# Optimization experiments

Measured on AMD Instinct MI355X. Metric: run time of the kernel, lower is better.

The kernel has to match this reference:

```python
import jax, jax.numpy as jnp
import numpy as np

NUM_EMBEDDINGS = 8192
EMBEDDING_DIM = 512
COMMITMENT_COST = 0.25
N_INPUTS = 32768


def setup_inputs() -> dict:
    key = jax.random.key(0)
    k1, k2 = jax.random.split(key)
    inputs = jax.random.normal(k1, (N_INPUTS, EMBEDDING_DIM), dtype=jnp.float32)
    weight = jax.random.normal(k2, (NUM_EMBEDDINGS, EMBEDDING_DIM), dtype=jnp.float32)
    return {"inputs": inputs, "weight": weight}


def reference(inputs, weight):
    # distances[n, k] = ||x_n||^2 + ||w_k||^2 - 2 x_n . w_k   -> [N, K]
    distances = (
        jnp.sum(inputs ** 2, axis=1, keepdims=True)
        + jnp.sum(weight ** 2, axis=1)
        - 2.0 * (inputs @ weight.T)
    )
    probs = jax.nn.softmax(-distances, axis=-1)            # [N, K]
    idx = jnp.argmin(distances, axis=1)                    # [N]
    quantized = weight[idx]                                # gather == one-hot @ weight

    e_latent_loss = jnp.mean((jax.lax.stop_gradient(quantized) - inputs) ** 2)
    q_latent_loss = jnp.mean((quantized - jax.lax.stop_gradient(inputs)) ** 2)
    loss = q_latent_loss + COMMITMENT_COST * e_latent_loss

    # straight-through estimator
    quantized_st = inputs + jax.lax.stop_gradient(quantized - inputs)

    # avg over one-hot encodings == normalized code histogram
    counts = jnp.bincount(idx, length=NUM_EMBEDDINGS).astype(inputs.dtype)
    avg_probs = counts / inputs.shape[0]
    perplexity = jnp.exp(-jnp.sum(avg_probs * jnp.log(avg_probs + 1e-10)))

    return (quantized_st, probs, loss, perplexity)
```

## Files before the change

### kernel.cpp

```cpp
#include <hip/hip_runtime.h>
#include <hip/hip_fp16.h>
#include <math.h>

#define N_ROWS 32768
#define K_CODES 8192
#define DIM 512

#define OUT_Q 0
#define OUT_P ((size_t)N_ROWS * DIM)
#define OUT_LOSS (OUT_P + (size_t)N_ROWS * K_CODES)
#define OUT_PERP (OUT_LOSS + 1)

#define WS_WSQ 0
#define WS_CNT (K_CODES)
#define WS_ERR (2 * K_CODES)
#define WS_F16 (2 * K_CODES + N_ROWS)

#define XH_OFF ((size_t)0)
#define XL_OFF ((size_t)N_ROWS * DIM)
#define WH_OFF ((size_t)2 * N_ROWS * DIM)
#define WL_OFF ((size_t)2 * N_ROWS * DIM + (size_t)K_CODES * DIM)
#define F16_COUNT ((size_t)2 * (N_ROWS + K_CODES) * DIM)
#define WS_NEEDED ((size_t)WS_F16 * 4 + F16_COUNT * 2)

typedef _Float16 f16x8 __attribute__((ext_vector_type(8)));
typedef float f32x4 __attribute__((ext_vector_type(4)));

__device__ inline void load_lds16(const void* g, void* l) {
    __builtin_amdgcn_global_load_lds((const __attribute__((address_space(1))) void*)g,
                                     (__attribute__((address_space(3))) void*)l,
                                     16, 0, 0);
}

__device__ inline unsigned int fkey(float f) {
    unsigned int b = __float_as_uint(f);
    return b ^ ((unsigned int)((int)b >> 31) | 0x80000000u);
}
__device__ inline float fkey_inv(unsigned int k) {
    unsigned int b = (k & 0x80000000u) ? (k ^ 0x80000000u) : ~k;
    return __uint_as_float(b);
}

__global__ void wsq_kernel(const float* __restrict__ W, float* __restrict__ ws) {
    int row = blockIdx.x;
    int lane = threadIdx.x;
    const float* src = W + (size_t)row * DIM;
    float4 v0 = *(const float4*)(src + lane * 8);
    float4 v1 = *(const float4*)(src + lane * 8 + 4);
    float s = v0.x * v0.x + v0.y * v0.y + v0.z * v0.z + v0.w * v0.w
            + v1.x * v1.x + v1.y * v1.y + v1.z * v1.z + v1.w * v1.w;
#pragma unroll
    for (int off = 32; off > 0; off >>= 1) s += __shfl_down(s, off, 64);
    if (lane == 0) ws[WS_WSQ + row] = s;
}

__global__ void __launch_bounds__(256) convert_split_kernel(
    const float* __restrict__ X, const float* __restrict__ W,
    _Float16* __restrict__ f16base) {
    const size_t NX8 = (size_t)N_ROWS * DIM / 8;
    size_t t = (size_t)blockIdx.x * 256 + threadIdx.x;
    const float* src;
    _Float16 *hd, *ld;
    if (t < NX8) {
        src = X + t * 8;
        hd = f16base + XH_OFF + t * 8;
        ld = f16base + XL_OFF + t * 8;
    } else {
        size_t u = t - NX8;
        src = W + u * 8;
        hd = f16base + WH_OFF + u * 8;
        ld = f16base + WL_OFF + u * 8;
    }
    float4 v0 = *(const float4*)src;
    float4 v1 = *(const float4*)(src + 4);
    float v[8] = {v0.x, v0.y, v0.z, v0.w, v1.x, v1.y, v1.z, v1.w};
    f16x8 h, l;
#pragma unroll
    for (int i = 0; i < 8; ++i) {
        _Float16 hv = (_Float16)v[i];
        h[i] = hv;
        l[i] = (_Float16)(v[i] - (float)hv);
    }
    *(f16x8*)hd = h;
    *(f16x8*)ld = l;
}

__global__ void __launch_bounds__(256) gemm_dist_mfma_kernel(
    const _Float16* __restrict__ f16base, const float* __restrict__ ws,
    float* __restrict__ out) {
    __shared__ _Float16 lds[4][128][32];

    const int tid = threadIdx.x;
    const int w = tid >> 6;
    const int lane = tid & 63;
    const int bn = blockIdx.x * 128;
    const int bm = blockIdx.y * 128;
    const int wr = w >> 1;
    const int wc = w & 1;

    const _Float16* src_base;
    int tile_row_base;
    if (w == 0)      { src_base = f16base + XH_OFF; tile_row_base = bm; }
    else if (w == 1) { src_base = f16base + XL_OFF; tile_row_base = bm; }
    else if (w == 2) { src_base = f16base + WH_OFF; tile_row_base = bn; }
    else             { src_base = f16base + WL_OFF; tile_row_base = bn; }

    const int lrow = lane >> 2;
    const int p = lane & 3;

    f32x4 acc[4][4];
#pragma unroll
    for (int i = 0; i < 4; ++i)
#pragma unroll
        for (int j = 0; j < 4; ++j) acc[i][j] = (f32x4){0.f, 0.f, 0.f, 0.f};

    const int q = lane >> 4;
    const int fm = lane & 15;

    for (int k0 = 0; k0 < DIM; k0 += 32) {
        __syncthreads();
#pragma unroll
        for (int e = 0; e < 8; ++e) {
            int m = e * 16 + lrow;
            int c = p ^ ((m >> 1) & 3);
            const _Float16* gp =
                src_base + (size_t)(tile_row_base + m) * DIM + k0 + c * 8;
            load_lds16(gp, &lds[w][e * 16][0]);
        }
        __syncthreads();

        f16x8 ah[4], al[4], bh[4], bl[4];
#pragma unroll
        for (int i = 0; i < 4; ++i) {
            int am = wr * 64 + i * 16 + fm;
            int sa = (am >> 1) & 3;
            ah[i] = *(const f16x8*)&lds[0][am][(q ^ sa) * 8];
            al[i] = *(const f16x8*)&lds[1][am][(q ^ sa) * 8];
            int bb = wc * 64 + i * 16 + fm;
            int sb = (bb >> 1) & 3;
            bh[i] = *(const f16x8*)&lds[2][bb][(q ^ sb) * 8];
            bl[i] = *(const f16x8*)&lds[3][bb][(q ^ sb) * 8];
        }
#pragma unroll
        for (int i = 0; i < 4; ++i)
#pragma unroll
            for (int j = 0; j < 4; ++j) {
                acc[i][j] = __builtin_amdgcn_mfma_f32_16x16x32_f16(
                    ah[i], bh[j], acc[i][j], 0, 0, 0);
                acc[i][j] = __builtin_amdgcn_mfma_f32_16x16x32_f16(
                    ah[i], bl[j], acc[i][j], 0, 0, 0);
                acc[i][j] = __builtin_amdgcn_mfma_f32_16x16x32_f16(
                    al[i], bh[j], acc[i][j], 0, 0, 0);
            }
    }

    const float* wsq = ws + WS_WSQ;
    float* Dout = out + OUT_P;
    const int q4 = (lane >> 4) * 4;
#pragma unroll
    for (int i = 0; i < 4; ++i) {
#pragma unroll
        for (int j = 0; j < 4; ++j) {
            int n = bn + wc * 64 + j * 16 + fm;
            float wn = wsq[n];
#pragma unroll
            for (int r = 0; r < 4; ++r) {
                int m = bm + wr * 64 + i * 16 + q4 + r;
                Dout[(size_t)m * K_CODES + n] = wn - 2.f * acc[i][j][r];
            }
        }
    }
}

#define BM 128
#define BN 128
#define BK 16

__global__ void __launch_bounds__(256) gemm_dist_fp32_kernel(
    const float* __restrict__ X, const float* __restrict__ W,
    const float* __restrict__ ws, float* __restrict__ out) {
    __shared__ float As[BK][BM];
    __shared__ float Bs[BK][BN];

    const int bn = blockIdx.x * BN;
    const int bm = blockIdx.y * BM;
    const int tid = threadIdx.x;
    const int tx = tid & 15;
    const int ty = tid >> 4;
    const int lr = tid >> 1;
    const int lc = (tid & 1) * 8;

    float acc[8][8];
#pragma unroll
    for (int i = 0; i < 8; ++i)
#pragma unroll
        for (int j = 0; j < 8; ++j) acc[i][j] = 0.f;

    const float* aptr = X + (size_t)(bm + lr) * DIM + lc;
    const float* bptr = W + (size_t)(bn + lr) * DIM + lc;

    for (int k0 = 0; k0 < DIM; k0 += BK) {
        float4 a0 = *(const float4*)(aptr + k0);
        float4 a1 = *(const float4*)(aptr + k0 + 4);
        float4 b0 = *(const float4*)(bptr + k0);
        float4 b1 = *(const float4*)(bptr + k0 + 4);
        __syncthreads();
        As[lc + 0][lr] = a0.x; As[lc + 1][lr] = a0.y;
        As[lc + 2][lr] = a0.z; As[lc + 3][lr] = a0.w;
        As[lc + 4][lr] = a1.x; As[lc + 5][lr] = a1.y;
        As[lc + 6][lr] = a1.z; As[lc + 7][lr] = a1.w;
        Bs[lc + 0][lr] = b0.x; Bs[lc + 1][lr] = b0.y;
        Bs[lc + 2][lr] = b0.z; Bs[lc + 3][lr] = b0.w;
        Bs[lc + 4][lr] = b1.x; Bs[lc + 5][lr] = b1.y;
        Bs[lc + 6][lr] = b1.z; Bs[lc + 7][lr] = b1.w;
        __syncthreads();
#pragma unroll
        for (int kk = 0; kk < BK; ++kk) {
            float a[8], b[8];
            *(float4*)&a[0] = *(const float4*)&As[kk][ty * 8];
            *(float4*)&a[4] = *(const float4*)&As[kk][ty * 8 + 4];
            *(float4*)&b[0] = *(const float4*)&Bs[kk][tx * 8];
            *(float4*)&b[4] = *(const float4*)&Bs[kk][tx * 8 + 4];
#pragma unroll
            for (int i = 0; i < 8; ++i)
#pragma unroll
                for (int j = 0; j < 8; ++j)
                    acc[i][j] = fmaf(a[i], b[j], acc[i][j]);
        }
    }

    const float* wsq = ws + WS_WSQ;
    const int m0 = bm + ty * 8;
    const int n0 = bn + tx * 8;
    float wn[8];
    *(float4*)&wn[0] = *(const float4*)(wsq + n0);
    *(float4*)&wn[4] = *(const float4*)(wsq + n0 + 4);
    float* Dout = out + OUT_P;
#pragma unroll
    for (int i = 0; i < 8; ++i) {
        float4 o0, o1;
        o0.x = wn[0] - 2.f * acc[i][0];
        o0.y = wn[1] - 2.f * acc[i][1];
        o0.z = wn[2] - 2.f * acc[i][2];
        o0.w = wn[3] - 2.f * acc[i][3];
        o1.x = wn[4] - 2.f * acc[i][4];
        o1.y = wn[5] - 2.f * acc[i][5];
        o1.z = wn[6] - 2.f * acc[i][6];
        o1.w = wn[7] - 2.f * acc[i][7];
        float* drow = Dout + (size_t)(m0 + i) * K_CODES + n0;
        *(float4*)(drow) = o0;
        *(float4*)(drow + 4) = o1;
    }
}

__global__ void __launch_bounds__(256) probs_quant_kernel(
    const float* __restrict__ X, const float* __restrict__ W,
    float* __restrict__ out, float* __restrict__ ws) {
    const int n = blockIdx.x;
    const int tid = threadIdx.x;
    __shared__ unsigned long long mred[4];
    __shared__ float fred[4];

    float4* Drow4 = (float4*)(out + OUT_P + (size_t)n * K_CODES);

    float4 e[8];
    unsigned long long best = ~0ull;
#pragma unroll
    for (int t = 0; t < 8; ++t) {
        float4 v = Drow4[tid + t * 256];
        e[t] = v;
        unsigned int c0 = (unsigned int)((tid + t * 256) * 4);
        unsigned long long k;
        k = ((unsigned long long)fkey(v.x) << 32) | (c0 + 0u);
        best = k < best ? k : best;
        k = ((unsigned long long)fkey(v.y) << 32) | (c0 + 1u);
        best = k < best ? k : best;
        k = ((unsigned long long)fkey(v.z) << 32) | (c0 + 2u);
        best = k < best ? k : best;
        k = ((unsigned long long)fkey(v.w) << 32) | (c0 + 3u);
        best = k < best ? k : best;
    }
#pragma unroll
    for (int d = 1; d < 64; d <<= 1) {
        unsigned long long o = __shfl_xor(best, d, 64);
        best = o < best ? o : best;
    }
    if ((tid & 63) == 0) mred[tid >> 6] = best;
    __syncthreads();
    unsigned long long bm = mred[0];
    bm = mred[1] < bm ? mred[1] : bm;
    bm = mred[2] < bm ? mred[2] : bm;
    bm = mred[3] < bm ? mred[3] : bm;
    const float smin = fkey_inv((unsigned int)(bm >> 32));
    const int amin = (int)(bm & 0xFFFFFFFFu);

    float sum = 0.f;
#pragma unroll
    for (int t = 0; t < 8; ++t) {
        float4 v = e[t];
        float4 ev;
        ev.x = __expf(smin - v.x);
        ev.y = __expf(smin - v.y);
        ev.z = __expf(smin - v.z);
        ev.w = __expf(smin - v.w);
        e[t] = ev;
        sum += ev.x + ev.y + ev.z + ev.w;
    }
#pragma unroll
    for (int off = 32; off > 0; off >>= 1) sum += __shfl_down(sum, off, 64);
    if ((tid & 63) == 0) fred[tid >> 6] = sum;
    __syncthreads();
    const float inv = 1.0f / (fred[0] + fred[1] + fred[2] + fred[3]);

#pragma unroll
    for (int t = 0; t < 8; ++t) {
        float4 ev = e[t];
        ev.x *= inv; ev.y *= inv; ev.z *= inv; ev.w *= inv;
        Drow4[tid + t * 256] = ev;
    }

    const float2* xr = (const float2*)(X + (size_t)n * DIM);
    const float2* wr = (const float2*)(W + (size_t)amin * DIM);
    float2* qr = (float2*)(out + OUT_Q + (size_t)n * DIM);
    float2 x = xr[tid];
    float2 qv = wr[tid];
    float2 d2, o;
    d2.x = qv.x - x.x; d2.y = qv.y - x.y;
    o.x = x.x + d2.x;  o.y = x.y + d2.y;
    qr[tid] = o;
    float err = d2.x * d2.x + d2.y * d2.y;
#pragma unroll
    for (int off = 32; off > 0; off >>= 1) err += __shfl_down(err, off, 64);
    __syncthreads();
    if ((tid & 63) == 0) fred[tid >> 6] = err;
    __syncthreads();
    if (tid == 0) {
        ws[WS_ERR + n] = fred[0] + fred[1] + fred[2] + fred[3];
        atomicAdd(ws + WS_CNT + amin, 1.0f);
    }
}

__global__ void __launch_bounds__(256) finalize_kernel(
    float* __restrict__ out, const float* __restrict__ ws) {
    __shared__ float red[256];
    const int tid = threadIdx.x;

    float errsum = 0.f;
    for (int j = tid; j < N_ROWS; j += 256) errsum += ws[WS_ERR + j];
    red[tid] = errsum;
    __syncthreads();
    for (int st = 128; st > 0; st >>= 1) {
        if (tid < st) red[tid] += red[tid + st];
        __syncthreads();
    }
    const float total_err = red[0];
    __syncthreads();

    float ent = 0.f;
    for (int j = tid; j < K_CODES; j += 256) {
        float p = ws[WS_CNT + j] * (1.0f / (float)N_ROWS);
        ent -= p * logf(p + 1e-10f);
    }
    red[tid] = ent;
    __syncthreads();
    for (int st = 128; st > 0; st >>= 1) {
        if (tid < st) red[tid] += red[tid + st];
        __syncthreads();
    }
    if (tid == 0) {
        float mse = total_err * (1.0f / ((float)N_ROWS * (float)DIM));
        out[OUT_LOSS] = mse + 0.25f * mse;
        out[OUT_PERP] = expf(red[0]);
    }
}

extern "C" void kernel_launch(void* const* d_in, const int* in_sizes, int n_in,
                              void* d_out, int out_size, void* d_ws, size_t ws_size,
                              hipStream_t stream) {
    const float* X = (const float*)d_in[0];
    const float* W = (const float*)d_in[1];
    float* out = (float*)d_out;
    float* ws = (float*)d_ws;

    hipMemsetAsync(ws + WS_CNT, 0, K_CODES * sizeof(float), stream);

    wsq_kernel<<<K_CODES, 64, 0, stream>>>(W, ws);

    if (ws_size >= WS_NEEDED) {
        _Float16* f16base = (_Float16*)(ws + WS_F16);
        const int conv_blocks =
            (int)(((size_t)(N_ROWS + K_CODES) * DIM / 8 + 255) / 256);
        convert_split_kernel<<<conv_blocks, 256, 0, stream>>>(X, W, f16base);

        dim3 ggrid(K_CODES / 128, N_ROWS / 128);
        gemm_dist_mfma_kernel<<<ggrid, 256, 0, stream>>>(f16base, ws, out);
    } else {
        dim3 ggrid(K_CODES / BN, N_ROWS / BM);
        gemm_dist_fp32_kernel<<<ggrid, 256, 0, stream>>>(X, W, ws, out);
    }

    probs_quant_kernel<<<N_ROWS, 256, 0, stream>>>(X, W, out, ws);
    finalize_kernel<<<1, 256, 0, stream>>>(out, ws);
}
```

Before: 2.445 ms.

## Triple-buffer the split-fp16 MFMA GEMM with 256x128 tiles and fuse wsq into conversion

The distance GEMM now uses 512-thread blocks computing 256x128 tiles. A three-stage LDS ring prefetches two K-steps ahead, with explicit vmcnt waits, split barriers, setprio around the MFMA bursts, and a swizzled block order for L2 reuse. The codebook squared-norm reduction moves into the fp32-to-fp16 split kernel, removing a separate launch, and finalize uses 1024 threads. The cost is more hand scheduling, more LDS per block, and reliance on exact counts of outstanding loads.

Measured after the change: 2.311 ms. 5.5% less time.

```diff
diff --git a/kernel.cpp b/kernel.cpp
--- a/kernel.cpp
+++ b/kernel.cpp
@@ -56,12 +56,13 @@
 
 __global__ void __launch_bounds__(256) convert_split_kernel(
     const float* __restrict__ X, const float* __restrict__ W,
-    _Float16* __restrict__ f16base) {
+    _Float16* __restrict__ f16base, float* __restrict__ ws) {
     const size_t NX8 = (size_t)N_ROWS * DIM / 8;
     size_t t = (size_t)blockIdx.x * 256 + threadIdx.x;
     const float* src;
     _Float16 *hd, *ld;
-    if (t < NX8) {
+    bool isW = (t >= NX8);
+    if (!isW) {
         src = X + t * 8;
         hd = f16base + XH_OFF + t * 8;
         ld = f16base + XL_OFF + t * 8;
@@ -75,88 +76,153 @@
     float4 v1 = *(const float4*)(src + 4);
     float v[8] = {v0.x, v0.y, v0.z, v0.w, v1.x, v1.y, v1.z, v1.w};
     f16x8 h, l;
+    float s = 0.f;
 #pragma unroll
     for (int i = 0; i < 8; ++i) {
         _Float16 hv = (_Float16)v[i];
         h[i] = hv;
         l[i] = (_Float16)(v[i] - (float)hv);
+        s += v[i] * v[i];
     }
     *(f16x8*)hd = h;
     *(f16x8*)ld = l;
-}
-
-__global__ void __launch_bounds__(256) gemm_dist_mfma_kernel(
+    if (isW) {
+#pragma unroll
+        for (int off = 32; off > 0; off >>= 1) s += __shfl_down(s, off, 64);
+        if ((threadIdx.x & 63) == 0) ws[WS_WSQ + ((t - NX8) >> 6)] = s;
+    }
+}
+
+#define LDSB 24576
+#define AH_O 0
+#define AL_O 8192
+#define BH_O 16384
+#define BL_O 20480
+
+__global__ void __launch_bounds__(512, 2) gemm_dist_mfma_kernel(
     const _Float16* __restrict__ f16base, const float* __restrict__ ws,
     float* __restrict__ out) {
-    __shared__ _Float16 lds[4][128][32];
+    __shared__ _Float16 lds[3 * LDSB];
 
     const int tid = threadIdx.x;
     const int w = tid >> 6;
     const int lane = tid & 63;
-    const int bn = blockIdx.x * 128;
-    const int bm = blockIdx.y * 128;
+
+    int lin = blockIdx.y * 64 + blockIdx.x;
+    int swz = (lin & 7) * 1024 + (lin >> 3);
+    const int bn = (swz & 63) * 128;
+    const int bm = (swz >> 6) * 256;
+
     const int wr = w >> 1;
     const int wc = w & 1;
-
-    const _Float16* src_base;
-    int tile_row_base;
-    if (w == 0)      { src_base = f16base + XH_OFF; tile_row_base = bm; }
-    else if (w == 1) { src_base = f16base + XL_OFF; tile_row_base = bm; }
-    else if (w == 2) { src_base = f16base + WH_OFF; tile_row_base = bn; }
-    else             { src_base = f16base + WL_OFF; tile_row_base = bn; }
-
-    const int lrow = lane >> 2;
-    const int p = lane & 3;
-
-    f32x4 acc[4][4];
-#pragma unroll
-    for (int i = 0; i < 4; ++i)
-#pragma unroll
-        for (int j = 0; j < 4; ++j) acc[i][j] = (f32x4){0.f, 0.f, 0.f, 0.f};
-
     const int q = lane >> 4;
     const int fm = lane & 15;
-
-    for (int k0 = 0; k0 < DIM; k0 += 32) {
-        __syncthreads();
-#pragma unroll
-        for (int e = 0; e < 8; ++e) {
-            int m = e * 16 + lrow;
-            int c = p ^ ((m >> 1) & 3);
-            const _Float16* gp =
-                src_base + (size_t)(tile_row_base + m) * DIM + k0 + c * 8;
-            load_lds16(gp, &lds[w][e * 16][0]);
-        }
-        __syncthreads();
-
-        f16x8 ah[4], al[4], bh[4], bl[4];
-#pragma unroll
-        for (int i = 0; i < 4; ++i) {
+    const int l4 = lane >> 2;
+    const int p = lane & 3;
+
+    f32x4 acc[4][4];
+#pragma unroll
+    for (int i = 0; i < 4; ++i)
+#pragma unroll
+        for (int j = 0; j < 4; ++j) acc[i][j] = (f32x4){0.f, 0.f, 0.f, 0.f};
+
+    auto stage = [&](int ks, _Float16* buf, int part) {
+        const int kk = ks * 32;
+        int g = w * 2 + part;
+        int arow = g * 16 + l4;
+        int ca = p ^ ((arow >> 1) & 3);
+        size_t aoff = (size_t)(bm + arow) * DIM + kk + ca * 8;
+        load_lds16(f16base + XH_OFF + aoff, buf + AH_O + g * 512);
+        load_lds16(f16base + XL_OFF + aoff, buf + AL_O + g * 512);
+        int brow = w * 16 + l4;
+        int cb = p ^ ((brow >> 1) & 3);
+        size_t boff = (size_t)(bn + brow) * DIM + kk + cb * 8;
+        if (part == 0)
+            load_lds16(f16base + WH_OFF + boff, buf + BH_O + w * 512);
+        else
+            load_lds16(f16base + WL_OFF + boff, buf + BL_O + w * 512);
+    };
+
+    _Float16* c0 = lds;
+    _Float16* c1 = lds + LDSB;
+    _Float16* c2 = lds + 2 * LDSB;
+
+    stage(0, c0, 0); stage(0, c0, 1);
+    stage(1, c1, 0); stage(1, c1, 1);
+    asm volatile("s_waitcnt vmcnt(6)" ::: "memory");
+    __builtin_amdgcn_s_barrier();
+    __builtin_amdgcn_sched_barrier(0);
+
+#pragma unroll 1
+    for (int ks = 0; ks < 16; ++ks) {
+        f16x8 bhv[4], blv[4];
+#pragma unroll
+        for (int j = 0; j < 4; ++j) {
+            int bb = wc * 64 + j * 16 + fm;
+            int off = bb * 32 + ((q ^ ((bb >> 1) & 3)) * 8);
+            bhv[j] = *(const f16x8*)&c0[BH_O + off];
+            blv[j] = *(const f16x8*)&c0[BL_O + off];
+        }
+        f16x8 ah[2], al[2];
+#pragma unroll
+        for (int i = 0; i < 2; ++i) {
             int am = wr * 64 + i * 16 + fm;
-            int sa = (am >> 1) & 3;
-            ah[i] = *(const f16x8*)&lds[0][am][(q ^ sa) * 8];
-            al[i] = *(const f16x8*)&lds[1][am][(q ^ sa) * 8];
-            int bb = wc * 64 + i * 16 + fm;
-            int sb = (bb >> 1) & 3;
-            bh[i] = *(const f16x8*)&lds[2][bb][(q ^ sb) * 8];
-            bl[i] = *(const f16x8*)&lds[3][bb][(q ^ sb) * 8];
-        }
-#pragma unroll
-        for (int i = 0; i < 4; ++i)
+            int off = am * 32 + ((q ^ ((am >> 1) & 3)) * 8);
+            ah[i] = *(const f16x8*)&c0[AH_O + off];
+            al[i] = *(const f16x8*)&c0[AL_O + off];
+        }
+        if (ks < 14) stage(ks + 2, c2, 0);
+        __builtin_amdgcn_s_setprio(1);
+#pragma unroll
+        for (int i = 0; i < 2; ++i)
 #pragma unroll
             for (int j = 0; j < 4; ++j) {
                 acc[i][j] = __builtin_amdgcn_mfma_f32_16x16x32_f16(
-                    ah[i], bh[j], acc[i][j], 0, 0, 0);
+                    ah[i], bhv[j], acc[i][j], 0, 0, 0);
                 acc[i][j] = __builtin_amdgcn_mfma_f32_16x16x32_f16(
-                    ah[i], bl[j], acc[i][j], 0, 0, 0);
+                    ah[i], blv[j], acc[i][j], 0, 0, 0);
                 acc[i][j] = __builtin_amdgcn_mfma_f32_16x16x32_f16(
-                    al[i], bh[j], acc[i][j], 0, 0, 0);
+                    al[i], bhv[j], acc[i][j], 0, 0, 0);
             }
+        __builtin_amdgcn_s_setprio(0);
+        __builtin_amdgcn_s_barrier();
+        __builtin_amdgcn_sched_barrier(0);
+
+#pragma unroll
+        for (int i = 0; i < 2; ++i) {
+            int am = wr * 64 + (i + 2) * 16 + fm;
+            int off = am * 32 + ((q ^ ((am >> 1) & 3)) * 8);
+            ah[i] = *(const f16x8*)&c0[AH_O + off];
+            al[i] = *(const f16x8*)&c0[AL_O + off];
+        }
+        if (ks < 14) stage(ks + 2, c2, 1);
+        __builtin_amdgcn_s_setprio(1);
+#pragma unroll
+        for (int i = 0; i < 2; ++i)
+#pragma unroll
+            for (int j = 0; j < 4; ++j) {
+                acc[i + 2][j] = __builtin_amdgcn_mfma_f32_16x16x32_f16(
+                    ah[i], bhv[j], acc[i + 2][j], 0, 0, 0);
+                acc[i + 2][j] = __builtin_amdgcn_mfma_f32_16x16x32_f16(
+                    ah[i], blv[j], acc[i + 2][j], 0, 0, 0);
+                acc[i + 2][j] = __builtin_amdgcn_mfma_f32_16x16x32_f16(
+                    al[i], bhv[j], acc[i + 2][j], 0, 0, 0);
+            }
+        __builtin_amdgcn_s_setprio(0);
+        if (ks < 14) {
+            asm volatile("s_waitcnt vmcnt(6)" ::: "memory");
+        } else if (ks == 14) {
+            asm volatile("s_waitcnt vmcnt(0)" ::: "memory");
+        }
+        __builtin_amdgcn_s_barrier();
+        __builtin_amdgcn_sched_barrier(0);
+
+        _Float16* t0 = c0; c0 = c1; c1 = c2; c2 = t0;
     }
 
     const float* wsq = ws + WS_WSQ;
     float* Dout = out + OUT_P;
-    const int q4 = (lane >> 4) * 4;
+    const int q4 = q * 4;
 #pragma unroll
     for (int i = 0; i < 4; ++i) {
 #pragma unroll
@@ -340,16 +406,16 @@
     }
 }
 
-__global__ void __launch_bounds__(256) finalize_kernel(
+__global__ void __launch_bounds__(1024) finalize_kernel(
     float* __restrict__ out, const float* __restrict__ ws) {
-    __shared__ float red[256];
+    __shared__ float red[1024];
     const int tid = threadIdx.x;
 
     float errsum = 0.f;
-    for (int j = tid; j < N_ROWS; j += 256) errsum += ws[WS_ERR + j];
+    for (int j = tid; j < N_ROWS; j += 1024) errsum += ws[WS_ERR + j];
     red[tid] = errsum;
     __syncthreads();
-    for (int st = 128; st > 0; st >>= 1) {
+    for (int st = 512; st > 0; st >>= 1) {
         if (tid < st) red[tid] += red[tid + st];
         __syncthreads();
     }
@@ -357,13 +423,13 @@
     __syncthreads();
 
     float ent = 0.f;
-    for (int j = tid; j < K_CODES; j += 256) {
+    for (int j = tid; j < K_CODES; j += 1024) {
         float p = ws[WS_CNT + j] * (1.0f / (float)N_ROWS);
         ent -= p * logf(p + 1e-10f);
     }
     red[tid] = ent;
     __syncthreads();
-    for (int st = 128; st > 0; st >>= 1) {
+    for (int st = 512; st > 0; st >>= 1) {
         if (tid < st) red[tid] += red[tid + st];
         __syncthreads();
     }
@@ -384,21 +450,20 @@
 
     hipMemsetAsync(ws + WS_CNT, 0, K_CODES * sizeof(float), stream);
 
-    wsq_kernel<<<K_CODES, 64, 0, stream>>>(W, ws);
-
     if (ws_size >= WS_NEEDED) {
         _Float16* f16base = (_Float16*)(ws + WS_F16);
         const int conv_blocks =
             (int)(((size_t)(N_ROWS + K_CODES) * DIM / 8 + 255) / 256);
-        convert_split_kernel<<<conv_blocks, 256, 0, stream>>>(X, W, f16base);
-
-        dim3 ggrid(K_CODES / 128, N_ROWS / 128);
-        gemm_dist_mfma_kernel<<<ggrid, 256, 0, stream>>>(f16base, ws, out);
+        convert_split_kernel<<<conv_blocks, 256, 0, stream>>>(X, W, f16base, ws);
+
+        dim3 ggrid(64, 128);
+        gemm_dist_mfma_kernel<<<ggrid, 512, 0, stream>>>(f16base, ws, out);
     } else {
+        wsq_kernel<<<K_CODES, 64, 0, stream>>>(W, ws);
         dim3 ggrid(K_CODES / BN, N_ROWS / BM);
         gemm_dist_fp32_kernel<<<ggrid, 256, 0, stream>>>(X, W, ws, out);
     }
 
     probs_quant_kernel<<<N_ROWS, 256, 0, stream>>>(X, W, out, ws);
-    finalize_kernel<<<1, 256, 0, stream>>>(out, ws);
-}
+    finalize_kernel<<<1, 1024, 0, stream>>>(out, ws);
+}
```
